# Performance work log

Measured on AMD Instinct MI355X. Metric: run time of the kernel, lower is better.

Reference implementation:

```python
import jax, jax.numpy as jnp
import numpy as np

N_NODES = 50000
N_EDGES = 600000
IN_FEATS = 128
N_HIDDEN = 128
N_CLASSES = 40


def setup_inputs() -> dict:
    key = jax.random.key(0)
    ks = jax.random.split(key, 12)
    feat = jax.random.normal(ks[0], (N_NODES, IN_FEATS), dtype=jnp.float32)
    src = jax.random.randint(ks[1], (N_EDGES,), 0, N_NODES, dtype=jnp.int32)
    dst = jax.random.randint(ks[2], (N_EDGES,), 0, N_NODES, dtype=jnp.int32)
    dims = [(IN_FEATS, N_HIDDEN), (N_HIDDEN, N_HIDDEN), (N_HIDDEN, N_CLASSES)]
    params = {}
    for i, (di, do) in enumerate(dims):
        s = 1.0 / np.sqrt(di)
        params[f"w_self{i}"] = jax.random.uniform(ks[3 + 3 * i], (di, do), jnp.float32, -s, s)
        params[f"w_neigh{i}"] = jax.random.uniform(ks[4 + 3 * i], (di, do), jnp.float32, -s, s)
        params[f"b{i}"] = jnp.zeros((do,), jnp.float32)
    return dict(feat=feat, src=src, dst=dst, **params)


def _sage_layer(h, src, dst, w_self, w_neigh, b):
    # mean aggregation over in-neighbors: msg = h[src], reduce at dst
    msg_sum = jax.ops.segment_sum(h[src], dst, num_segments=N_NODES)  # [N, d]
    deg = jax.ops.segment_sum(jnp.ones((src.shape[0],), h.dtype), dst, num_segments=N_NODES)
    h_neigh = msg_sum / jnp.maximum(deg, 1.0)[:, None]
    # DGL SAGEConv(mean): out = fc_self(h) + fc_neigh(mean_neigh) + bias
    return h @ w_self + h_neigh @ w_neigh + b


def reference(feat, src, dst,
              w_self0, w_neigh0, b0,
              w_self1, w_neigh1, b1,
              w_self2, w_neigh2, b2):
    # dropout p=0.0 -> identity
    h = _sage_layer(feat, src, dst, w_self0, w_neigh0, b0)
    h = jax.nn.relu(h)
    h = _sage_layer(h, src, dst, w_self1, w_neigh1, b1)
    h = jax.nn.relu(h)
    h = _sage_layer(h, src, dst, w_self2, w_neigh2, b2)
    return h
```

## Files before the change

### kernel.cpp

```cpp
#include <hip/hip_runtime.h>

#define N_NODES 50000
#define N_EDGES 600000

typedef short bf16x8 __attribute__((ext_vector_type(8)));
typedef float f32x4  __attribute__((ext_vector_type(4)));
typedef unsigned short u16x8 __attribute__((ext_vector_type(8)));
typedef unsigned short u16x4 __attribute__((ext_vector_type(4)));

__device__ inline ushort rne_bf16(float a) {
    union { float f; unsigned u; } v; v.f = a;
    return (ushort)((v.u + 0x7FFFu + ((v.u >> 16) & 1u)) >> 16);
}
__device__ inline float bf16_to_f32(ushort h) {
    return __uint_as_float((unsigned)h << 16);
}
__device__ inline void split_bf16(float a, ushort& hi, ushort& lo) {
    hi = rne_bf16(a);
    float hv = bf16_to_f32(hi);
    lo = rne_bf16(a - hv);
}


__global__ void count_deg_kernel(const int* __restrict__ dst, int* __restrict__ deg, int ne) {
    int e = blockIdx.x * blockDim.x + threadIdx.x;
    if (e < ne) atomicAdd(&deg[dst[e]], 1);
}

__global__ __launch_bounds__(256) void block_sums_kernel(const int* __restrict__ deg,
                                                         int* __restrict__ bsum, int n) {
    __shared__ int s[256];
    int t = threadIdx.x;
    int i = blockIdx.x * 256 + t;
    s[t] = (i < n) ? deg[i] : 0;
    __syncthreads();
    #pragma unroll
    for (int d = 128; d > 0; d >>= 1) {
        if (t < d) s[t] += s[t + d];
        __syncthreads();
    }
    if (t == 0) bsum[blockIdx.x] = s[0];
}

__global__ __launch_bounds__(256) void scatter_fused_kernel(const int* __restrict__ deg,
                                                            const int* __restrict__ bsum,
                                                            int* __restrict__ off,
                                                            int* __restrict__ cur,
                                                            int n, int nb) {
    __shared__ int s[256];
    int t = threadIdx.x;

    int bv = (t < nb) ? bsum[t] : 0;
    s[t] = bv;
    __syncthreads();
    #pragma unroll
    for (int d = 1; d < 256; d <<= 1) {
        int x = (t >= d) ? s[t - d] : 0;
        __syncthreads();
        s[t] += x;
        __syncthreads();
    }
    int base = (blockIdx.x > 0) ? s[blockIdx.x - 1] : 0;
    if (blockIdx.x == 0 && t == 0) off[n] = s[255];
    __syncthreads();

    int i = blockIdx.x * 256 + t;
    int v = (i < n) ? deg[i] : 0;
    s[t] = v;
    __syncthreads();
    #pragma unroll
    for (int d = 1; d < 256; d <<= 1) {
        int x = (t >= d) ? s[t - d] : 0;
        __syncthreads();
        s[t] += x;
        __syncthreads();
    }
    if (i < n) {
        int excl = s[t] - v + base;
        off[i] = excl;
        cur[i] = excl;
    }
}

__global__ void fill_csr_kernel(const int* __restrict__ src, const int* __restrict__ dst,
                                int* __restrict__ cur, int* __restrict__ ssrc, int ne) {
    int e = blockIdx.x * blockDim.x + threadIdx.x;
    if (e < ne) {
        int p = atomicAdd(&cur[dst[e]], 1);
        ssrc[p] = src[e];
    }
}

__global__ void convert_all_w(const float* __restrict__ ws0, const float* __restrict__ wn0,
                              const float* __restrict__ ws1, const float* __restrict__ wn1,
                              const float* __restrict__ ws2, const float* __restrict__ wn2,
                              ushort* __restrict__ Bth0, ushort* __restrict__ Btl0,
                              ushort* __restrict__ Bth1, ushort* __restrict__ Btl1,
                              ushort* __restrict__ Bth2, ushort* __restrict__ Btl2) {
    int b = blockIdx.x;
    int k = threadIdx.x;
    const float *Ws, *Wn;
    ushort *H, *L;
    int dout, n;
    if (b < 256)      { n = b;       dout = 128; Ws = ws0; Wn = wn0; H = Bth0; L = Btl0; }
    else if (b < 512) { n = b - 256; dout = 128; Ws = ws1; Wn = wn1; H = Bth1; L = Btl1; }
    else              { n = b - 512; dout = 40;  Ws = ws2; Wn = wn2; H = Bth2; L = Btl2; }
    float w = (n < dout) ? Ws[(long)k * dout + n] : Wn[(long)k * dout + (n - dout)];
    ushort hi, lo;
    split_bf16(w, hi, lo);
    H[n * 128 + k] = hi;
    L[n * 128 + k] = lo;
}


#define KDIM 128
#define APAD 136

__device__ inline void load_a16(const float* __restrict__ A, int grow, int M, int seg,
                                float* __restrict__ f) {
    if (grow < M) {
        const float* ap = A + (long)grow * KDIM + seg;
        #pragma unroll
        for (int q = 0; q < 4; ++q) {
            float4 a = *(const float4*)(ap + q * 4);
            f[q * 4 + 0] = a.x; f[q * 4 + 1] = a.y;
            f[q * 4 + 2] = a.z; f[q * 4 + 3] = a.w;
        }
    } else {
        #pragma unroll
        for (int i = 0; i < 16; ++i) f[i] = 0.f;
    }
}

__device__ inline void split_store16(const float* __restrict__ f,
                                     ushort* __restrict__ Ahi, ushort* __restrict__ Alo,
                                     int m, int seg) {
    ushort h[16], l[16];
    #pragma unroll
    for (int i = 0; i < 16; ++i) split_bf16(f[i], h[i], l[i]);
    #pragma unroll
    for (int q = 0; q < 2; ++q) {
        uint4 hw, lw;
        hw.x = (unsigned)h[q*8+0] | ((unsigned)h[q*8+1] << 16);
        hw.y = (unsigned)h[q*8+2] | ((unsigned)h[q*8+3] << 16);
        hw.z = (unsigned)h[q*8+4] | ((unsigned)h[q*8+5] << 16);
        hw.w = (unsigned)h[q*8+6] | ((unsigned)h[q*8+7] << 16);
        lw.x = (unsigned)l[q*8+0] | ((unsigned)l[q*8+1] << 16);
        lw.y = (unsigned)l[q*8+2] | ((unsigned)l[q*8+3] << 16);
        lw.z = (unsigned)l[q*8+4] | ((unsigned)l[q*8+5] << 16);
        lw.w = (unsigned)l[q*8+6] | ((unsigned)l[q*8+7] << 16);
        *(uint4*)&Ahi[m * APAD + seg + q * 8] = hw;
        *(uint4*)&Alo[m * APAD + seg + q * 8] = lw;
    }
}

__global__ __launch_bounds__(256, 3) void gemm_mfma_wide(
    const float* __restrict__ A,
    const ushort* __restrict__ Bth, const ushort* __restrict__ Btl,
    const float* __restrict__ bias,
    float* __restrict__ S, ushort* __restrict__ T, int M)
{
    __shared__ ushort AhiB[2][32 * APAD];
    __shared__ ushort AloB[2][32 * APAD];

    const int tid = threadIdx.x;
    const int wave = tid >> 6;
    const int lane = tid & 63;
    const int lane16 = lane & 15;
    const int quad = lane >> 4;
    const int half = blockIdx.x & 1;
    const int colbase = half * 128 + wave * 32;
    const int ntiles = (M + 31) >> 5;
    const int bstride = gridDim.x >> 1;
    const int m   = tid >> 3;
    const int seg = (tid & 7) * 16;

    bf16x8 Bh[4][2], Bl[4][2];
    #pragma unroll
    for (int c = 0; c < 4; ++c) {
        #pragma unroll
        for (int ct = 0; ct < 2; ++ct) {
            const long boff = (long)(colbase + 16 * ct + lane16) * KDIM + c * 32 + quad * 8;
            Bh[c][ct] = *(const bf16x8*)(Bth + boff);
            Bl[c][ct] = *(const bf16x8*)(Btl + boff);
        }
    }
    f32x4 bv[2] = {};
    if (half == 0) {
        #pragma unroll
        for (int ct = 0; ct < 2; ++ct)
            bv[ct] = *(const f32x4*)(bias + wave * 32 + 16 * ct + quad * 4);
    }

    int rt = blockIdx.x >> 1;
    if (rt >= ntiles) return;

    float fa[16];
    load_a16(A, rt * 32 + m, M, seg, fa);
    split_store16(fa, &AhiB[0][0], &AloB[0][0], m, seg);
    __syncthreads();

    int cur = 0;
    while (true) {
        const int nrt = rt + bstride;
        float fn[16];
        if (nrt < ntiles) load_a16(A, nrt * 32 + m, M, seg, fn);

        const ushort* AH = &AhiB[cur][0];
        const ushort* AL = &AloB[cur][0];

        f32x4 acc[2][2] = {};
        #pragma unroll
        for (int c = 0; c < 4; ++c) {
            const int k0 = c * 32 + quad * 8;
            bf16x8 ah[2], al[2];
            #pragma unroll
            for (int r = 0; r < 2; ++r) {
                const int off = (16 * r + lane16) * APAD + k0;
                ah[r] = *(const bf16x8*)&AH[off];
                al[r] = *(const bf16x8*)&AL[off];
            }
            #pragma unroll
            for (int ct = 0; ct < 2; ++ct) {
                #pragma unroll
                for (int r = 0; r < 2; ++r) {
                    acc[r][ct] = __builtin_amdgcn_mfma_f32_16x16x32_bf16(Bh[c][ct], ah[r], acc[r][ct], 0, 0, 0);
                    acc[r][ct] = __builtin_amdgcn_mfma_f32_16x16x32_bf16(Bl[c][ct], ah[r], acc[r][ct], 0, 0, 0);
                    acc[r][ct] = __builtin_amdgcn_mfma_f32_16x16x32_bf16(Bh[c][ct], al[r], acc[r][ct], 0, 0, 0);
                }
            }
        }

        #pragma unroll
        for (int ct = 0; ct < 2; ++ct) {
            const int colL = wave * 32 + 16 * ct + quad * 4;
            #pragma unroll
            for (int r = 0; r < 2; ++r) {
                const int row = rt * 32 + 16 * r + lane16;
                if (row < M) {
                    if (half == 0) {
                        *(f32x4*)(S + (long)row * 128 + colL) = acc[r][ct] + bv[ct];
                    } else {
                        u16x4 t4;
                        #pragma unroll
                        for (int i = 0; i < 4; ++i) t4[i] = rne_bf16(acc[r][ct][i]);
                        *(u16x4*)(T + (long)row * 128 + colL) = t4;
                    }
                }
            }
        }

        if (nrt >= ntiles) break;
        split_store16(fn, &AhiB[cur ^ 1][0], &AloB[cur ^ 1][0], m, seg);
        __syncthreads();
        cur ^= 1;
        rt = nrt;
    }
}

__global__ __launch_bounds__(256, 2) void gemm_mfma_narrow(
    const float* __restrict__ A,
    const ushort* __restrict__ Bth, const ushort* __restrict__ Btl,
    const float* __restrict__ bias,
    float* __restrict__ S, ushort* __restrict__ T, int M)
{
    __shared__ ushort AhiB[2][32 * APAD];
    __shared__ ushort AloB[2][32 * APAD];

    const int tid = threadIdx.x;
    const int wave = tid >> 6;
    const int lane = tid & 63;
    const int lane16 = lane & 15;
    const int quad = lane >> 4;
    const int rtw = wave & 1;
    const int cg = wave >> 1;
    const int ctbase = cg * 3;
    const int nct = cg ? 2 : 3;
    const int ntiles = (M + 31) >> 5;
    const int m   = tid >> 3;
    const int seg = (tid & 7) * 16;

    bf16x8 Bh[4][3], Bl[4][3];
    #pragma unroll
    for (int c = 0; c < 4; ++c) {
        #pragma unroll
        for (int j = 0; j < 3; ++j) {
            if (j < nct) {
                const long boff = (long)(16 * (ctbase + j) + lane16) * KDIM + c * 32 + quad * 8;
                Bh[c][j] = *(const bf16x8*)(Bth + boff);
                Bl[c][j] = *(const bf16x8*)(Btl + boff);
            }
        }
    }

    int rt = blockIdx.x;
    if (rt >= ntiles) return;

    float fa[16];
    load_a16(A, rt * 32 + m, M, seg, fa);
    split_store16(fa, &AhiB[0][0], &AloB[0][0], m, seg);
    __syncthreads();

    int cur = 0;
    while (true) {
        const int nrt = rt + gridDim.x;
        float fn[16];
        if (nrt < ntiles) load_a16(A, nrt * 32 + m, M, seg, fn);

        const ushort* AH = &AhiB[cur][0];
        const ushort* AL = &AloB[cur][0];

        f32x4 acc[3] = {};
        #pragma unroll
        for (int c = 0; c < 4; ++c) {
            const int off = (rtw * 16 + lane16) * APAD + c * 32 + quad * 8;
            bf16x8 ah = *(const bf16x8*)&AH[off];
            bf16x8 al = *(const bf16x8*)&AL[off];
            #pragma unroll
            for (int j = 0; j < 3; ++j) {
                if (j < nct) {
                    acc[j] = __builtin_amdgcn_mfma_f32_16x16x32_bf16(Bh[c][j], ah, acc[j], 0, 0, 0);
                    acc[j] = __builtin_amdgcn_mfma_f32_16x16x32_bf16(Bl[c][j], ah, acc[j], 0, 0, 0);
                    acc[j] = __builtin_amdgcn_mfma_f32_16x16x32_bf16(Bh[c][j], al, acc[j], 0, 0, 0);
                }
            }
        }

        const int row = rt * 32 + rtw * 16 + lane16;
        #pragma unroll
        for (int j = 0; j < 3; ++j) {
            if (j < nct && row < M) {
                const int col0 = 16 * (ctbase + j) + quad * 4;
                if (col0 < 40) {
                    f32x4 bvv = *(const f32x4*)(bias + col0);
                    *(f32x4*)(S + (long)row * 40 + col0) = acc[j] + bvv;
                } else {
                    u16x4 t4;
                    #pragma unroll
                    for (int i = 0; i < 4; ++i) t4[i] = rne_bf16(acc[j][i]);
                    *(u16x4*)(T + (long)row * 40 + (col0 - 40)) = t4;
                }
            }
        }

        if (nrt >= ntiles) break;
        split_store16(fn, &AhiB[cur ^ 1][0], &AloB[cur ^ 1][0], m, seg);
        __syncthreads();
        cur ^= 1;
        rt = nrt;
    }
}


template <int RELU>
__global__ __launch_bounds__(256) void agg128_kernel(
    const float* __restrict__ S, const ushort* __restrict__ T,
    const int* __restrict__ off, const int* __restrict__ ssrc,
    float* __restrict__ out, int nnodes)
{
    const int node = (blockIdx.x * 256 + threadIdx.x) >> 6;
    if (node >= nnodes) return;
    const int lane = threadIdx.x & 63;
    const int slot = lane >> 4;
    const int col8 = (lane & 15) * 8;

    const int a = off[node];
    const int b = off[node + 1];

    f32x4 acc0a = {0,0,0,0}, acc0b = {0,0,0,0};
    f32x4 acc1a = {0,0,0,0}, acc1b = {0,0,0,0};

    int i = a;
    for (; i + 8 <= b; i += 8) {
        int s0 = ssrc[i + slot];
        int s1 = ssrc[i + 4 + slot];
        u16x8 v0 = *(const u16x8*)(T + (long)s0 * 128 + col8);
        u16x8 v1 = *(const u16x8*)(T + (long)s1 * 128 + col8);
        #pragma unroll
        for (int j = 0; j < 4; ++j) {
            acc0a[j] += bf16_to_f32(v0[j]);
            acc0b[j] += bf16_to_f32(v0[4 + j]);
            acc1a[j] += bf16_to_f32(v1[j]);
            acc1b[j] += bf16_to_f32(v1[4 + j]);
        }
    }
    for (; i < b; i += 4) {
        int e = i + slot;
        if (e < b) {
            int s = ssrc[e];
            u16x8 v = *(const u16x8*)(T + (long)s * 128 + col8);
            #pragma unroll
            for (int j = 0; j < 4; ++j) {
                acc0a[j] += bf16_to_f32(v[j]);
                acc0b[j] += bf16_to_f32(v[4 + j]);
            }
        }
    }
    f32x4 accA = acc0a + acc1a;
    f32x4 accB = acc0b + acc1b;

    #pragma unroll
    for (int m = 16; m <= 32; m <<= 1) {
        #pragma unroll
        for (int j = 0; j < 4; ++j) {
            accA[j] += __shfl_xor((float)accA[j], m);
            accB[j] += __shfl_xor((float)accB[j], m);
        }
    }

    if (slot == 0) {
        int deg = b - a;
        float scale = (deg > 0) ? (1.0f / (float)deg) : 0.f;
        f32x4 sA = *(const f32x4*)(S + (long)node * 128 + col8);
        f32x4 sB = *(const f32x4*)(S + (long)node * 128 + col8 + 4);
        f32x4 rA = sA + accA * scale;
        f32x4 rB = sB + accB * scale;
        if (RELU) {
            #pragma unroll
            for (int j = 0; j < 4; ++j) {
                rA[j] = fmaxf(rA[j], 0.f);
                rB[j] = fmaxf(rB[j], 0.f);
            }
        }
        *(f32x4*)(out + (long)node * 128 + col8) = rA;
        *(f32x4*)(out + (long)node * 128 + col8 + 4) = rB;
    }
}

template <int RELU>
__global__ __launch_bounds__(256) void agg40_kernel(
    const float* __restrict__ S, const ushort* __restrict__ T,
    const int* __restrict__ off, const int* __restrict__ ssrc,
    float* __restrict__ out, int nnodes)
{
    const int node = (blockIdx.x * 256 + threadIdx.x) >> 6;
    if (node >= nnodes) return;
    const int lane = threadIdx.x & 63;
    const bool active = lane < 60;
    const int slot = active ? (lane / 10) : 5;
    const int fi = lane % 10;
    const int fo = fi * 4;

    const int a = off[node];
    const int b = off[node + 1];

    f32x4 acc0 = {0,0,0,0}, acc1 = {0,0,0,0};

    int i = a;
    for (; i + 12 <= b; i += 12) {
        int s0 = ssrc[i + slot];
        int s1 = ssrc[i + 6 + slot];
        u16x4 v0 = *(const u16x4*)(T + (long)s0 * 40 + fo);
        u16x4 v1 = *(const u16x4*)(T + (long)s1 * 40 + fo);
        if (active) {
            #pragma unroll
            for (int j = 0; j < 4; ++j) {
                acc0[j] += bf16_to_f32(v0[j]);
                acc1[j] += bf16_to_f32(v1[j]);
            }
        }
    }
    for (; i < b; i += 6) {
        int e = i + slot;
        if (active && e < b) {
            int s = ssrc[e];
            u16x4 v = *(const u16x4*)(T + (long)s * 40 + fo);
            #pragma unroll
            for (int j = 0; j < 4; ++j) acc0[j] += bf16_to_f32(v[j]);
        }
    }
    f32x4 acc = acc0 + acc1;

    f32x4 tot = acc;
    #pragma unroll
    for (int d = 10; d <= 50; d += 10) {
        int srcl = fi + d;
        #pragma unroll
        for (int j = 0; j < 4; ++j) tot[j] += __shfl((float)acc[j], srcl);
    }

    if (lane < 10) {
        int deg = b - a;
        float scale = (deg > 0) ? (1.0f / (float)deg) : 0.f;
        f32x4 s4 = *(const f32x4*)(S + (long)node * 40 + fo);
        f32x4 r = s4 + tot * scale;
        if (RELU) {
            #pragma unroll
            for (int j = 0; j < 4; ++j) r[j] = fmaxf(r[j], 0.f);
        }
        *(f32x4*)(out + (long)node * 40 + fo) = r;
    }
}


extern "C" void kernel_launch(void* const* d_in, const int* in_sizes, int n_in,
                              void* d_out, int out_size, void* d_ws, size_t ws_size,
                              hipStream_t stream) {
    const float* feat = (const float*)d_in[0];
    const int*   src  = (const int*)d_in[1];
    const int*   dst  = (const int*)d_in[2];
    const float* ws0  = (const float*)d_in[3];
    const float* wn0  = (const float*)d_in[4];
    const float* b0   = (const float*)d_in[5];
    const float* ws1  = (const float*)d_in[6];
    const float* wn1  = (const float*)d_in[7];
    const float* b1   = (const float*)d_in[8];
    const float* ws2  = (const float*)d_in[9];
    const float* wn2  = (const float*)d_in[10];
    const float* b2   = (const float*)d_in[11];

    const int N = N_NODES;
    const int NE = N_EDGES;
    const int NB = (N + 255) / 256;

    char* ws = (char*)d_ws;
    int*    offsets = (int*)(ws + 0);
    int*    cursor  = (int*)(ws + 200704);
    int*    degi    = (int*)(ws + 401408);
    int*    bsum    = (int*)(ws + 601600);
    int*    ssrc    = (int*)(ws + 603648);
    ushort* Bth0 = (ushort*)(ws + 200704);
    ushort* Btl0 = (ushort*)(ws + 266240);
    ushort* Bth1 = (ushort*)(ws + 331776);
    ushort* Btl1 = (ushort*)(ws + 397312);
    ushort* Bth2 = (ushort*)(ws + 462848);
    ushort* Btl2 = (ushort*)(ws + 483328);
    float*  hbuf = (float*)(ws + 3003904);
    float*  sbuf = (float*)(ws + 28603904);
    ushort* tbuf = (ushort*)(ws + 54203904);

    hipMemsetAsync(degi, 0, (size_t)N * sizeof(int), stream);
    count_deg_kernel<<<(NE + 255) / 256, 256, 0, stream>>>(dst, degi, NE);
    block_sums_kernel<<<NB, 256, 0, stream>>>(degi, bsum, N);
    scatter_fused_kernel<<<NB, 256, 0, stream>>>(degi, bsum, offsets, cursor, N, NB);
    fill_csr_kernel<<<(NE + 255) / 256, 256, 0, stream>>>(src, dst, cursor, ssrc, NE);

    convert_all_w<<<592, 128, 0, stream>>>(ws0, wn0, ws1, wn1, ws2, wn2,
                                           Bth0, Btl0, Bth1, Btl1, Bth2, Btl2);

    const int gw = 768;
    const int gn = 512;
    const int ga = (N + 3) / 4;

    gemm_mfma_wide<<<gw, 256, 0, stream>>>(feat, Bth0, Btl0, b0, sbuf, tbuf, N);
    agg128_kernel<1><<<ga, 256, 0, stream>>>(sbuf, tbuf, offsets, ssrc, hbuf, N);

    gemm_mfma_wide<<<gw, 256, 0, stream>>>(hbuf, Bth1, Btl1, b1, sbuf, tbuf, N);
    agg128_kernel<1><<<ga, 256, 0, stream>>>(sbuf, tbuf, offsets, ssrc, hbuf, N);

    gemm_mfma_narrow<<<gn, 256, 0, stream>>>(hbuf, Bth2, Btl2, b2, sbuf, tbuf, N);
    agg40_kernel<0><<<ga, 256, 0, stream>>>(sbuf, tbuf, offsets, ssrc, (float*)d_out, N);
}
```

Measured before the change: 290.0 us.

## Fuse CSR build into GEMM launch and pass pre-split bf16 activations between layers

Degree counting and weight hi/lo conversion now share one grid-strided prep kernel. The CSR fill runs in dedicated blocks of the first GEMM launch, overlapping with the layer-0 matmul that does not need it. The aggregation kernels apply ReLU and write activations already split into bf16 hi/lo planes, so the next GEMM copies them straight into LDS without converting. Converted weights are staged in the output buffer as scratch. Together these cut kernel launches and repeated split arithmetic, at the cost of coupling unrelated work in one grid and relying on the output buffer being free until the last kernel.

```diff
diff --git a/kernel.cpp b/kernel.cpp
--- a/kernel.cpp
+++ b/kernel.cpp
@@ -2,6 +2,9 @@
 
 #define N_NODES 50000
 #define N_EDGES 600000
+#define NBLK    196
+#define KDIM    128
+#define APAD    136
 
 typedef short bf16x8 __attribute__((ext_vector_type(8)));
 typedef float f32x4  __attribute__((ext_vector_type(4)));
@@ -21,10 +24,35 @@
     lo = rne_bf16(a - hv);
 }
 
-
-__global__ void count_deg_kernel(const int* __restrict__ dst, int* __restrict__ deg, int ne) {
-    int e = blockIdx.x * blockDim.x + threadIdx.x;
-    if (e < ne) atomicAdd(&deg[dst[e]], 1);
+__global__ __launch_bounds__(256) void k_prep(
+    const int* __restrict__ dst, int* __restrict__ degi,
+    const float* __restrict__ ws0, const float* __restrict__ wn0,
+    const float* __restrict__ ws1, const float* __restrict__ wn1,
+    const float* __restrict__ ws2, const float* __restrict__ wn2,
+    ushort* __restrict__ Bth0, ushort* __restrict__ Btl0,
+    ushort* __restrict__ Bth1, ushort* __restrict__ Btl1,
+    ushort* __restrict__ Bth2, ushort* __restrict__ Btl2)
+{
+    const int b = blockIdx.x, t = threadIdx.x;
+    if (b < 192) {
+        for (int e = b * 256 + t; e < N_EDGES; e += 192 * 256)
+            atomicAdd(&degi[dst[e]], 1);
+    } else {
+        for (int i = (b - 192) * 256 + t; i < 592 * 128; i += 64 * 256) {
+            int bb = i >> 7, k = i & 127;
+            const float *Ws, *Wn;
+            ushort *H, *L;
+            int dout, n;
+            if (bb < 256)      { n = bb;       dout = 128; Ws = ws0; Wn = wn0; H = Bth0; L = Btl0; }
+            else if (bb < 512) { n = bb - 256; dout = 128; Ws = ws1; Wn = wn1; H = Bth1; L = Btl1; }
+            else               { n = bb - 512; dout = 40;  Ws = ws2; Wn = wn2; H = Bth2; L = Btl2; }
+            float w = (n < dout) ? Ws[(long)k * dout + n] : Wn[(long)k * dout + (n - dout)];
+            ushort hi, lo;
+            split_bf16(w, hi, lo);
+            H[n * 128 + k] = hi;
+            L[n * 128 + k] = lo;
+        }
+    }
 }
 
 __global__ __launch_bounds__(256) void block_sums_kernel(const int* __restrict__ deg,
@@ -82,42 +110,8 @@
     }
 }
 
-__global__ void fill_csr_kernel(const int* __restrict__ src, const int* __restrict__ dst,
-                                int* __restrict__ cur, int* __restrict__ ssrc, int ne) {
-    int e = blockIdx.x * blockDim.x + threadIdx.x;
-    if (e < ne) {
-        int p = atomicAdd(&cur[dst[e]], 1);
-        ssrc[p] = src[e];
-    }
-}
-
-__global__ void convert_all_w(const float* __restrict__ ws0, const float* __restrict__ wn0,
-                              const float* __restrict__ ws1, const float* __restrict__ wn1,
-                              const float* __restrict__ ws2, const float* __restrict__ wn2,
-                              ushort* __restrict__ Bth0, ushort* __restrict__ Btl0,
-                              ushort* __restrict__ Bth1, ushort* __restrict__ Btl1,
-                              ushort* __restrict__ Bth2, ushort* __restrict__ Btl2) {
-    int b = blockIdx.x;
-    int k = threadIdx.x;
-    const float *Ws, *Wn;
-    ushort *H, *L;
-    int dout, n;
-    if (b < 256)      { n = b;       dout = 128; Ws = ws0; Wn = wn0; H = Bth0; L = Btl0; }
-    else if (b < 512) { n = b - 256; dout = 128; Ws = ws1; Wn = wn1; H = Bth1; L = Btl1; }
-    else              { n = b - 512; dout = 40;  Ws = ws2; Wn = wn2; H = Bth2; L = Btl2; }
-    float w = (n < dout) ? Ws[(long)k * dout + n] : Wn[(long)k * dout + (n - dout)];
-    ushort hi, lo;
-    split_bf16(w, hi, lo);
-    H[n * 128 + k] = hi;
-    L[n * 128 + k] = lo;
-}
-
-
-#define KDIM 128
-#define APAD 136
-
-__device__ inline void load_a16(const float* __restrict__ A, int grow, int M, int seg,
-                                float* __restrict__ f) {
+__device__ __forceinline__ void load_a16(const float* __restrict__ A, int grow, int M, int seg,
+                                         float* __restrict__ f) {
     if (grow < M) {
         const float* ap = A + (long)grow * KDIM + seg;
         #pragma unroll
@@ -132,9 +126,9 @@
     }
 }
 
-__device__ inline void split_store16(const float* __restrict__ f,
-                                     ushort* __restrict__ Ahi, ushort* __restrict__ Alo,
-                                     int m, int seg) {
+__device__ __forceinline__ void split_store16(const float* __restrict__ f,
+                                              ushort* __restrict__ Ahi, ushort* __restrict__ Alo,
+                                              int m, int seg) {
     ushort h[16], l[16];
     #pragma unroll
     for (int i = 0; i < 16; ++i) split_bf16(f[i], h[i], l[i]);
@@ -154,8 +148,154 @@
     }
 }
 
-__global__ __launch_bounds__(256, 3) void gemm_mfma_wide(
+__device__ __forceinline__ void load_pl(const ushort* __restrict__ Phi, const ushort* __restrict__ Plo,
+                                        int grow, int M, int seg, uint4* __restrict__ r) {
+    if (grow < M) {
+        const uint4* ph = (const uint4*)(Phi + (long)grow * KDIM + seg);
+        const uint4* pl = (const uint4*)(Plo + (long)grow * KDIM + seg);
+        r[0] = ph[0]; r[1] = ph[1];
+        r[2] = pl[0]; r[3] = pl[1];
+    } else {
+        uint4 z = {0, 0, 0, 0};
+        r[0] = r[1] = r[2] = r[3] = z;
+    }
+}
+
+__device__ __forceinline__ void store_pl(const uint4* __restrict__ r,
+                                         ushort* __restrict__ Ahi, ushort* __restrict__ Alo,
+                                         int m, int seg) {
+    *(uint4*)&Ahi[m * APAD + seg] = r[0];
+    *(uint4*)&Ahi[m * APAD + seg + 8] = r[1];
+    *(uint4*)&Alo[m * APAD + seg] = r[2];
+    *(uint4*)&Alo[m * APAD + seg + 8] = r[3];
+}
+
+#define WIDE_MFMA_TILE()                                                                      \
+    f32x4 acc[2][2] = {};                                                                     \
+    _Pragma("unroll")                                                                         \
+    for (int c = 0; c < 4; ++c) {                                                             \
+        const int k0 = c * 32 + quad * 8;                                                     \
+        bf16x8 ah[2], al[2];                                                                  \
+        _Pragma("unroll")                                                                     \
+        for (int r = 0; r < 2; ++r) {                                                         \
+            const int off = (16 * r + lane16) * APAD + k0;                                    \
+            ah[r] = *(const bf16x8*)&AH[off];                                                 \
+            al[r] = *(const bf16x8*)&AL[off];                                                 \
+        }                                                                                     \
+        _Pragma("unroll")                                                                     \
+        for (int ct = 0; ct < 2; ++ct) {                                                      \
+            _Pragma("unroll")                                                                 \
+            for (int r = 0; r < 2; ++r) {                                                     \
+                acc[r][ct] = __builtin_amdgcn_mfma_f32_16x16x32_bf16(Bh[c][ct], ah[r], acc[r][ct], 0, 0, 0); \
+                acc[r][ct] = __builtin_amdgcn_mfma_f32_16x16x32_bf16(Bl[c][ct], ah[r], acc[r][ct], 0, 0, 0); \
+                acc[r][ct] = __builtin_amdgcn_mfma_f32_16x16x32_bf16(Bh[c][ct], al[r], acc[r][ct], 0, 0, 0); \
+            }                                                                                 \
+        }                                                                                     \
+    }
+
+#define WIDE_STORE_TILE()                                                                     \
+    _Pragma("unroll")                                                                         \
+    for (int ct = 0; ct < 2; ++ct) {                                                          \
+        const int colL = wave * 32 + 16 * ct + quad * 4;                                      \
+        _Pragma("unroll")                                                                     \
+        for (int r = 0; r < 2; ++r) {                                                         \
+            const int row = rt * 32 + 16 * r + lane16;                                        \
+            if (row < M) {                                                                    \
+                if (half == 0) {                                                              \
+                    *(f32x4*)(S + (long)row * 128 + colL) = acc[r][ct] + bv[ct];              \
+                } else {                                                                      \
+                    u16x4 t4;                                                                 \
+                    _Pragma("unroll")                                                         \
+                    for (int i = 0; i < 4; ++i) t4[i] = rne_bf16(acc[r][ct][i]);              \
+                    *(u16x4*)(T + (long)row * 128 + colL) = t4;                               \
+                }                                                                             \
+            }                                                                                 \
+        }                                                                                     \
+    }
+
+#define WIDE_B_PROLOGUE()                                                                     \
+    bf16x8 Bh[4][2], Bl[4][2];                                                                \
+    _Pragma("unroll")                                                                         \
+    for (int c = 0; c < 4; ++c) {                                                             \
+        _Pragma("unroll")                                                                     \
+        for (int ct = 0; ct < 2; ++ct) {                                                      \
+            const long boff = (long)(colbase + 16 * ct + lane16) * KDIM + c * 32 + quad * 8;  \
+            Bh[c][ct] = *(const bf16x8*)(Bth + boff);                                         \
+            Bl[c][ct] = *(const bf16x8*)(Btl + boff);                                         \
+        }                                                                                     \
+    }                                                                                         \
+    f32x4 bv[2] = {};                                                                         \
+    if (half == 0) {                                                                          \
+        _Pragma("unroll")                                                                     \
+        for (int ct = 0; ct < 2; ++ct)                                                        \
+            bv[ct] = *(const f32x4*)(bias + wave * 32 + 16 * ct + quad * 4);                  \
+    }
+
+__global__ __launch_bounds__(256, 3) void k_gemm_wide_f32_fill(
     const float* __restrict__ A,
+    const ushort* __restrict__ Bth, const ushort* __restrict__ Btl,
+    const float* __restrict__ bias,
+    float* __restrict__ S, ushort* __restrict__ T, int M,
+    const int* __restrict__ src, const int* __restrict__ dst,
+    int* __restrict__ cur, int* __restrict__ ssrcb)
+{
+    __shared__ ushort AhiB[2][32 * APAD];
+    __shared__ ushort AloB[2][32 * APAD];
+
+    if (blockIdx.x < 128) {
+        const int gtid = blockIdx.x * 256 + threadIdx.x;
+        for (int e = gtid; e < N_EDGES; e += 128 * 256) {
+            int p = atomicAdd(&cur[dst[e]], 1);
+            ssrcb[p] = src[e];
+        }
+        return;
+    }
+
+    const int bid = blockIdx.x - 128;
+    const int tid = threadIdx.x;
+    const int wave = tid >> 6;
+    const int lane = tid & 63;
+    const int lane16 = lane & 15;
+    const int quad = lane >> 4;
+    const int half = bid & 1;
+    const int colbase = half * 128 + wave * 32;
+    const int ntiles = (M + 31) >> 5;
+    const int bstride = 320;
+    const int m   = tid >> 3;
+    const int seg = (tid & 7) * 16;
+
+    WIDE_B_PROLOGUE();
+
+    int rt = bid >> 1;
+    if (rt >= ntiles) return;
+
+    float fa[16];
+    load_a16(A, rt * 32 + m, M, seg, fa);
+    split_store16(fa, &AhiB[0][0], &AloB[0][0], m, seg);
+    __syncthreads();
+
+    int cur_b = 0;
+    while (true) {
+        const int nrt = rt + bstride;
+        float fn[16];
+        if (nrt < ntiles) load_a16(A, nrt * 32 + m, M, seg, fn);
+
+        const ushort* AH = &AhiB[cur_b][0];
+        const ushort* AL = &AloB[cur_b][0];
+
+        WIDE_MFMA_TILE();
+        WIDE_STORE_TILE();
+
+        if (nrt >= ntiles) break;
+        split_store16(fn, &AhiB[cur_b ^ 1][0], &AloB[cur_b ^ 1][0], m, seg);
+        __syncthreads();
+        cur_b ^= 1;
+        rt = nrt;
+    }
+}
+
+__global__ __launch_bounds__(256, 3) void k_gemm_wide_pl(
+    const ushort* __restrict__ Phi, const ushort* __restrict__ Plo,
     const ushort* __restrict__ Bth, const ushort* __restrict__ Btl,
     const float* __restrict__ bias,
     float* __restrict__ S, ushort* __restrict__ T, int M)
@@ -175,91 +315,38 @@
     const int m   = tid >> 3;
     const int seg = (tid & 7) * 16;
 
-    bf16x8 Bh[4][2], Bl[4][2];
-    #pragma unroll
-    for (int c = 0; c < 4; ++c) {
-        #pragma unroll
-        for (int ct = 0; ct < 2; ++ct) {
-            const long boff = (long)(colbase + 16 * ct + lane16) * KDIM + c * 32 + quad * 8;
-            Bh[c][ct] = *(const bf16x8*)(Bth + boff);
-            Bl[c][ct] = *(const bf16x8*)(Btl + boff);
-        }
-    }
-    f32x4 bv[2] = {};
-    if (half == 0) {
-        #pragma unroll
-        for (int ct = 0; ct < 2; ++ct)
-            bv[ct] = *(const f32x4*)(bias + wave * 32 + 16 * ct + quad * 4);
-    }
+    WIDE_B_PROLOGUE();
 
     int rt = blockIdx.x >> 1;
     if (rt >= ntiles) return;
 
-    float fa[16];
-    load_a16(A, rt * 32 + m, M, seg, fa);
-    split_store16(fa, &AhiB[0][0], &AloB[0][0], m, seg);
+    uint4 ra[4];
+    load_pl(Phi, Plo, rt * 32 + m, M, seg, ra);
+    store_pl(ra, &AhiB[0][0], &AloB[0][0], m, seg);
     __syncthreads();
 
-    int cur = 0;
+    int cur_b = 0;
     while (true) {
         const int nrt = rt + bstride;
-        float fn[16];
-        if (nrt < ntiles) load_a16(A, nrt * 32 + m, M, seg, fn);
-
-        const ushort* AH = &AhiB[cur][0];
-        const ushort* AL = &AloB[cur][0];
-
-        f32x4 acc[2][2] = {};
-        #pragma unroll
-        for (int c = 0; c < 4; ++c) {
-            const int k0 = c * 32 + quad * 8;
-            bf16x8 ah[2], al[2];
-            #pragma unroll
-            for (int r = 0; r < 2; ++r) {
-                const int off = (16 * r + lane16) * APAD + k0;
-                ah[r] = *(const bf16x8*)&AH[off];
-                al[r] = *(const bf16x8*)&AL[off];
-            }
-            #pragma unroll
-            for (int ct = 0; ct < 2; ++ct) {
-                #pragma unroll
-                for (int r = 0; r < 2; ++r) {
-                    acc[r][ct] = __builtin_amdgcn_mfma_f32_16x16x32_bf16(Bh[c][ct], ah[r], acc[r][ct], 0, 0, 0);
-                    acc[r][ct] = __builtin_amdgcn_mfma_f32_16x16x32_bf16(Bl[c][ct], ah[r], acc[r][ct], 0, 0, 0);
-                    acc[r][ct] = __builtin_amdgcn_mfma_f32_16x16x32_bf16(Bh[c][ct], al[r], acc[r][ct], 0, 0, 0);
-                }
-            }
-        }
-
-        #pragma unroll
-        for (int ct = 0; ct < 2; ++ct) {
-            const int colL = wave * 32 + 16 * ct + quad * 4;
-            #pragma unroll
-            for (int r = 0; r < 2; ++r) {
-                const int row = rt * 32 + 16 * r + lane16;
-                if (row < M) {
-                    if (half == 0) {
-                        *(f32x4*)(S + (long)row * 128 + colL) = acc[r][ct] + bv[ct];
-                    } else {
-                        u16x4 t4;
-                        #pragma unroll
-                        for (int i = 0; i < 4; ++i) t4[i] = rne_bf16(acc[r][ct][i]);
-                        *(u16x4*)(T + (long)row * 128 + colL) = t4;
-                    }
-                }
-            }
-        }
+        uint4 rn[4];
+        if (nrt < ntiles) load_pl(Phi, Plo, nrt * 32 + m, M, seg, rn);
+
+        const ushort* AH = &AhiB[cur_b][0];
+        const ushort* AL = &AloB[cur_b][0];
+
+        WIDE_MFMA_TILE();
+        WIDE_STORE_TILE();
 
         if (nrt >= ntiles) break;
-        split_store16(fn, &AhiB[cur ^ 1][0], &AloB[cur ^ 1][0], m, seg);
-        __syncthreads();
-        cur ^= 1;
+        store_pl(rn, &AhiB[cur_b ^ 1][0], &AloB[cur_b ^ 1][0], m, seg);
+        __syncthreads();
+        cur_b ^= 1;
         rt = nrt;
     }
 }
 
-__global__ __launch_bounds__(256, 2) void gemm_mfma_narrow(
-    const float* __restrict__ A,
+__global__ __launch_bounds__(256, 2) void k_gemm_narrow_pl(
+    const ushort* __restrict__ Phi, const ushort* __restrict__ Plo,
     const ushort* __restrict__ Bth, const ushort* __restrict__ Btl,
     const float* __restrict__ bias,
     float* __restrict__ S, ushort* __restrict__ T, int M)
@@ -296,19 +383,19 @@
     int rt = blockIdx.x;
     if (rt >= ntiles) return;
 
-    float fa[16];
-    load_a16(A, rt * 32 + m, M, seg, fa);
-    split_store16(fa, &AhiB[0][0], &AloB[0][0], m, seg);
+    uint4 ra[4];
+    load_pl(Phi, Plo, rt * 32 + m, M, seg, ra);
+    store_pl(ra, &AhiB[0][0], &AloB[0][0], m, seg);
     __syncthreads();
 
-    int cur = 0;
+    int cur_b = 0;
     while (true) {
         const int nrt = rt + gridDim.x;
-        float fn[16];
-        if (nrt < ntiles) load_a16(A, nrt * 32 + m, M, seg, fn);
-
-        const ushort* AH = &AhiB[cur][0];
-        const ushort* AL = &AloB[cur][0];
+        uint4 rn[4];
+        if (nrt < ntiles) load_pl(Phi, Plo, nrt * 32 + m, M, seg, rn);
+
+        const ushort* AH = &AhiB[cur_b][0];
+        const ushort* AL = &AloB[cur_b][0];
 
         f32x4 acc[3] = {};
         #pragma unroll
@@ -344,19 +431,17 @@
         }
 
         if (nrt >= ntiles) break;
-        split_store16(fn, &AhiB[cur ^ 1][0], &AloB[cur ^ 1][0], m, seg);
-        __syncthreads();
-        cur ^= 1;
+        store_pl(rn, &AhiB[cur_b ^ 1][0], &AloB[cur_b ^ 1][0], m, seg);
+        __syncthreads();
+        cur_b ^= 1;
         rt = nrt;
     }
 }
 
-
-template <int RELU>
-__global__ __launch_bounds__(256) void agg128_kernel(
+__global__ __launch_bounds__(256) void k_agg128_pl(
     const float* __restrict__ S, const ushort* __restrict__ T,
-    const int* __restrict__ off, const int* __restrict__ ssrc,
-    float* __restrict__ out, int nnodes)
+    const int* __restrict__ off, const int* __restrict__ ssrcb,
+    ushort* __restrict__ Phi, ushort* __restrict__ Plo, int nnodes)
 {
     const int node = (blockIdx.x * 256 + threadIdx.x) >> 6;
     if (node >= nnodes) return;
@@ -372,8 +457,8 @@
 
     int i = a;
     for (; i + 8 <= b; i += 8) {
-        int s0 = ssrc[i + slot];
-        int s1 = ssrc[i + 4 + slot];
+        int s0 = ssrcb[i + slot];
+        int s1 = ssrcb[i + 4 + slot];
         u16x8 v0 = *(const u16x8*)(T + (long)s0 * 128 + col8);
         u16x8 v1 = *(const u16x8*)(T + (long)s1 * 128 + col8);
         #pragma unroll
@@ -387,7 +472,7 @@
     for (; i < b; i += 4) {
         int e = i + slot;
         if (e < b) {
-            int s = ssrc[e];
+            int s = ssrcb[e];
             u16x8 v = *(const u16x8*)(T + (long)s * 128 + col8);
             #pragma unroll
             for (int j = 0; j < 4; ++j) {
@@ -400,11 +485,11 @@
     f32x4 accB = acc0b + acc1b;
 
     #pragma unroll
-    for (int m = 16; m <= 32; m <<= 1) {
+    for (int mm = 16; mm <= 32; mm <<= 1) {
         #pragma unroll
         for (int j = 0; j < 4; ++j) {
-            accA[j] += __shfl_xor((float)accA[j], m);
-            accB[j] += __shfl_xor((float)accB[j], m);
+            accA[j] += __shfl_xor((float)accA[j], mm);
+            accB[j] += __shfl_xor((float)accB[j], mm);
         }
     }
 
@@ -415,22 +500,30 @@
         f32x4 sB = *(const f32x4*)(S + (long)node * 128 + col8 + 4);
         f32x4 rA = sA + accA * scale;
         f32x4 rB = sB + accB * scale;
-        if (RELU) {
-            #pragma unroll
-            for (int j = 0; j < 4; ++j) {
-                rA[j] = fmaxf(rA[j], 0.f);
-                rB[j] = fmaxf(rB[j], 0.f);
-            }
-        }
-        *(f32x4*)(out + (long)node * 128 + col8) = rA;
-        *(f32x4*)(out + (long)node * 128 + col8 + 4) = rB;
-    }
-}
-
-template <int RELU>
-__global__ __launch_bounds__(256) void agg40_kernel(
+        #pragma unroll
+        for (int j = 0; j < 4; ++j) {
+            rA[j] = fmaxf(rA[j], 0.f);
+            rB[j] = fmaxf(rB[j], 0.f);
+        }
+        u16x8 ph, pl;
+        #pragma unroll
+        for (int j = 0; j < 4; ++j) {
+            ushort h, l;
+            split_bf16(rA[j], h, l); ph[j] = h; pl[j] = l;
+        }
+        #pragma unroll
+        for (int j = 0; j < 4; ++j) {
+            ushort h, l;
+            split_bf16(rB[j], h, l); ph[4 + j] = h; pl[4 + j] = l;
+        }
+        *(u16x8*)(Phi + (long)node * 128 + col8) = ph;
+        *(u16x8*)(Plo + (long)node * 128 + col8) = pl;
+    }
+}
+
+__global__ __launch_bounds__(256) void k_agg40(
     const float* __restrict__ S, const ushort* __restrict__ T,
-    const int* __restrict__ off, const int* __restrict__ ssrc,
+    const int* __restrict__ off, const int* __restrict__ ssrcb,
     float* __restrict__ out, int nnodes)
 {
     const int node = (blockIdx.x * 256 + threadIdx.x) >> 6;
@@ -448,8 +541,8 @@
 
     int i = a;
     for (; i + 12 <= b; i += 12) {
-        int s0 = ssrc[i + slot];
-        int s1 = ssrc[i + 6 + slot];
+        int s0 = ssrcb[i + slot];
+        int s1 = ssrcb[i + 6 + slot];
         u16x4 v0 = *(const u16x4*)(T + (long)s0 * 40 + fo);
         u16x4 v1 = *(const u16x4*)(T + (long)s1 * 40 + fo);
         if (active) {
@@ -463,7 +556,7 @@
     for (; i < b; i += 6) {
         int e = i + slot;
         if (active && e < b) {
-            int s = ssrc[e];
+            int s = ssrcb[e];
             u16x4 v = *(const u16x4*)(T + (long)s * 40 + fo);
             #pragma unroll
             for (int j = 0; j < 4; ++j) acc0[j] += bf16_to_f32(v[j]);
@@ -484,10 +577,6 @@
         float scale = (deg > 0) ? (1.0f / (float)deg) : 0.f;
         f32x4 s4 = *(const f32x4*)(S + (long)node * 40 + fo);
         f32x4 r = s4 + tot * scale;
-        if (RELU) {
-            #pragma unroll
-            for (int j = 0; j < 4; ++j) r[j] = fmaxf(r[j], 0.f);
-        }
         *(f32x4*)(out + (long)node * 40 + fo) = r;
     }
 }
@@ -510,44 +599,42 @@
     const float* b2   = (const float*)d_in[11];
 
     const int N = N_NODES;
-    const int NE = N_EDGES;
-    const int NB = (N + 255) / 256;
 
     char* ws = (char*)d_ws;
     int*    offsets = (int*)(ws + 0);
     int*    cursor  = (int*)(ws + 200704);
     int*    degi    = (int*)(ws + 401408);
     int*    bsum    = (int*)(ws + 601600);
-    int*    ssrc    = (int*)(ws + 603648);
-    ushort* Bth0 = (ushort*)(ws + 200704);
-    ushort* Btl0 = (ushort*)(ws + 266240);
-    ushort* Bth1 = (ushort*)(ws + 331776);
-    ushort* Btl1 = (ushort*)(ws + 397312);
-    ushort* Bth2 = (ushort*)(ws + 462848);
-    ushort* Btl2 = (ushort*)(ws + 483328);
-    float*  hbuf = (float*)(ws + 3003904);
+    int*    ssrcb   = (int*)(ws + 603648);
+    ushort* Phi  = (ushort*)(ws + 3003904);
+    ushort* Plo  = (ushort*)(ws + 15803904);
     float*  sbuf = (float*)(ws + 28603904);
     ushort* tbuf = (ushort*)(ws + 54203904);
 
+    ushort* Ball = (ushort*)d_out;
+    ushort* Bth0 = Ball;
+    ushort* Btl0 = Ball + 32768;
+    ushort* Bth1 = Ball + 65536;
+    ushort* Btl1 = Ball + 98304;
+    ushort* Bth2 = Ball + 131072;
+    ushort* Btl2 = Ball + 141312;
+
     hipMemsetAsync(degi, 0, (size_t)N * sizeof(int), stream);
-    count_deg_kernel<<<(NE + 255) / 256, 256, 0, stream>>>(dst, degi, NE);
-    block_sums_kernel<<<NB, 256, 0, stream>>>(degi, bsum, N);
-    scatter_fused_kernel<<<NB, 256, 0, stream>>>(degi, bsum, offsets, cursor, N, NB);
-    fill_csr_kernel<<<(NE + 255) / 256, 256, 0, stream>>>(src, dst, cursor, ssrc, NE);
-
-    convert_all_w<<<592, 128, 0, stream>>>(ws0, wn0, ws1, wn1, ws2, wn2,
-                                           Bth0, Btl0, Bth1, Btl1, Bth2, Btl2);
-
-    const int gw = 768;
-    const int gn = 512;
+    k_prep<<<256, 256, 0, stream>>>(dst, degi, ws0, wn0, ws1, wn1, ws2, wn2,
+                                    Bth0, Btl0, Bth1, Btl1, Bth2, Btl2);
+
+    block_sums_kernel<<<NBLK, 256, 0, stream>>>(degi, bsum, N);
+    scatter_fused_kernel<<<NBLK, 256, 0, stream>>>(degi, bsum, offsets, cursor, N, NBLK);
+
     const int ga = (N + 3) / 4;
 
-    gemm_mfma_wide<<<gw, 256, 0, stream>>>(feat, Bth0, Btl0, b0, sbuf, tbuf, N);
-    agg128_kernel<1><<<ga, 256, 0, stream>>>(sbuf, tbuf, offsets, ssrc, hbuf, N);
-
-    gemm_mfma_wide<<<gw, 256, 0, stream>>>(hbuf, Bth1, Btl1, b1, sbuf, tbuf, N);
-    agg128_kernel<1><<<ga, 256, 0, stream>>>(sbuf, tbuf, offsets, ssrc, hbuf, N);
-
-    gemm_mfma_narrow<<<gn, 256, 0, stream>>>(hbuf, Bth2, Btl2, b2, sbuf, tbuf, N);
-    agg40_kernel<0><<<ga, 256, 0, stream>>>(sbuf, tbuf, offsets, ssrc, (float*)d_out, N);
-}
+    k_gemm_wide_f32_fill<<<768, 256, 0, stream>>>(feat, Bth0, Btl0, b0, sbuf, tbuf, N,
+                                                  src, dst, cursor, ssrcb);
+    k_agg128_pl<<<ga, 256, 0, stream>>>(sbuf, tbuf, offsets, ssrcb, Phi, Plo, N);
+
+    k_gemm_wide_pl<<<768, 256, 0, stream>>>(Phi, Plo, Bth1, Btl1, b1, sbuf, tbuf, N);
+    k_agg128_pl<<<ga, 256, 0, stream>>>(sbuf, tbuf, offsets, ssrcb, Phi, Plo, N);
+
+    k_gemm_narrow_pl<<<512, 256, 0, stream>>>(Phi, Plo, Bth2, Btl2, b2, sbuf, tbuf, N);
+    k_agg40<<<ga, 256, 0, stream>>>(sbuf, tbuf, offsets, ssrcb, (float*)d_out, N);
+}
```

Result: faster. 275.9 us (-4.9%).
